# Optimization experiments

Measured on AMD Instinct MI355X. Metric: run time of the kernel, lower is better.

The kernel has to match this reference:

```python
import jax, jax.numpy as jnp
import numpy as np

N = 2048
D_MODEL = 1024
N_HEADS = 16
D_HEAD = D_MODEL // N_HEADS


def setup_inputs() -> dict:
    key = jax.random.key(0)
    ks = jax.random.split(key, 12)
    s = 1.0 / np.sqrt(D_MODEL)
    inp = {
        "x": jax.random.normal(ks[0], (N, D_MODEL), dtype=jnp.float32),
        "edge_bias": jax.random.normal(ks[1], (N, N, N_HEADS), dtype=jnp.float32) * 0.1,
        # torch.nn.Linear convention: y = x @ W.T + b, W: [out, in]
        "Wq": jax.random.normal(ks[2], (D_MODEL, D_MODEL), dtype=jnp.float32) * s,
        "bq": jax.random.normal(ks[3], (D_MODEL,), dtype=jnp.float32) * s,
        "Wk": jax.random.normal(ks[4], (D_MODEL, D_MODEL), dtype=jnp.float32) * s,
        "bk": jax.random.normal(ks[5], (D_MODEL,), dtype=jnp.float32) * s,
        "Wv": jax.random.normal(ks[6], (D_MODEL, D_MODEL), dtype=jnp.float32) * s,
        "bv": jax.random.normal(ks[7], (D_MODEL,), dtype=jnp.float32) * s,
        "Wo": jax.random.normal(ks[8], (D_MODEL, D_MODEL), dtype=jnp.float32) * s,
        "bo": jax.random.normal(ks[9], (D_MODEL,), dtype=jnp.float32) * s,
    }
    return inp


def reference(x, edge_bias, Wq, bq, Wk, bk, Wv, bv, Wo, bo):
    # x: [N, d], edge_bias: [N, N, H]
    scale = D_HEAD ** -0.5
    q = (x @ Wq.T + bq).reshape(N, N_HEADS, D_HEAD)  # [N, H, Dh]
    k = (x @ Wk.T + bk).reshape(N, N_HEADS, D_HEAD)
    v = (x @ Wv.T + bv).reshape(N, N_HEADS, D_HEAD)
    # attn[h, i, j] = q_i . k_j * scale + edge_bias[i, j, h]
    attn = jnp.einsum("nhd,mhd->hnm", q, k) * scale
    attn = attn + jnp.transpose(edge_bias, (2, 0, 1))
    attn = jax.nn.softmax(attn, axis=-1)
    # dropout is identity in eval/reference mode
    out = jnp.einsum("hnm,mhd->nhd", attn, v).reshape(N, D_MODEL)
    return out @ Wo.T + bo
```

## Files before the change

kernel.cpp:

```cpp
#include <hip/hip_runtime.h>
#include <math.h>

#define NTOK 2048
#define DM   1024
#define NH   16
#define DH   64
#define GM   2048
#define GN   1024
#define GK   1024
#define SCALE 0.125f

typedef __attribute__((ext_vector_type(8))) short short8;
typedef __attribute__((ext_vector_type(4))) float floatx4;
typedef unsigned short ushort_t;

__device__ __forceinline__ unsigned short f2bf(float f) {
    unsigned u = __builtin_bit_cast(unsigned, f);
    u += 0x7fffu + ((u >> 16) & 1u);
    return (unsigned short)(u >> 16);
}

__global__ __launch_bounds__(256) void convert5(
    const float* __restrict__ x,  const float* __restrict__ wq,
    const float* __restrict__ wk, const float* __restrict__ wv,
    const float* __restrict__ wo, ushort_t* __restrict__ dst)
{
    const size_t i4 = (size_t)blockIdx.x * 256 + threadIdx.x;
    const float* src; size_t off;
    if      (i4 <  524288) { src = x;  off = 0;       }
    else if (i4 <  786432) { src = wq; off = 524288;  }
    else if (i4 < 1048576) { src = wk; off = 786432;  }
    else if (i4 < 1310720) { src = wv; off = 1048576; }
    else                   { src = wo; off = 1310720; }
    float4 v = ((const float4*)src)[i4 - off];
    ushort4 o;
    o.x = f2bf(v.x); o.y = f2bf(v.y); o.z = f2bf(v.z); o.w = f2bf(v.w);
    ((ushort4*)dst)[i4] = o;
}

template<int BM, int BN>
__global__ __launch_bounds__(256) void gemm_bt(
    const ushort_t* __restrict__ A,
    const ushort_t* __restrict__ B0, const ushort_t* __restrict__ B1,
    const ushort_t* __restrict__ B2,
    const float* __restrict__ bi0, const float* __restrict__ bi1,
    const float* __restrict__ bi2,
    void* C0, void* C1, void* C2, int mode0, int mode1, int mode2)
{
    constexpr int AC = BM * 4 / 256;
    constexpr int BC = BN * 4 / 256;
    constexpr int FI = BM / 32;
    constexpr int FJ = BN / 32;
    constexpr int WM = BM / 2;
    constexpr int WN = BN / 2;

    const int z = blockIdx.z;
    const ushort_t* B   = (z == 0) ? B0  : (z == 1) ? B1  : B2;
    const float*    bia = (z == 0) ? bi0 : (z == 1) ? bi1 : bi2;
    void*           C   = (z == 0) ? C0  : (z == 1) ? C1  : C2;
    const int mode      = (z == 0) ? mode0 : (z == 1) ? mode1 : mode2;

    __shared__ __align__(16) ushort_t As[BM][32];
    __shared__ __align__(16) ushort_t Bs[BN][32];

    const int t    = threadIdx.x;
    const int w    = t >> 6;
    const int L    = t & 63;
    const int r16  = L & 15;
    const int quad = L >> 4;
    const int wm   = w & 1;
    const int wn   = w >> 1;

    const int m0 = blockIdx.y * BM;
    const int n0 = blockIdx.x * BN;

    const int srow = t >> 2;
    const int skc  = (t & 3) * 8;

    const ushort_t* ap = A + (size_t)(m0 + srow) * GK + skc;
    const ushort_t* bp = B + (size_t)(n0 + srow) * GK + skc;

    floatx4 acc[FI][FJ];
#pragma unroll
    for (int i = 0; i < FI; ++i)
#pragma unroll
        for (int j = 0; j < FJ; ++j) acc[i][j] = (floatx4){0.f, 0.f, 0.f, 0.f};

    short8 areg[AC], breg[BC];
#pragma unroll
    for (int c = 0; c < AC; ++c) areg[c] = *(const short8*)(ap + (size_t)c * 64 * GK);
#pragma unroll
    for (int c = 0; c < BC; ++c) breg[c] = *(const short8*)(bp + (size_t)c * 64 * GK);

    for (int ks = 0; ks < GK / 32; ++ks) {
        __syncthreads();
#pragma unroll
        for (int c = 0; c < AC; ++c) *(short8*)&As[c * 64 + srow][skc] = areg[c];
#pragma unroll
        for (int c = 0; c < BC; ++c) *(short8*)&Bs[c * 64 + srow][skc] = breg[c];
        __syncthreads();
        if (ks < GK / 32 - 1) {
            ap += 32; bp += 32;
#pragma unroll
            for (int c = 0; c < AC; ++c) areg[c] = *(const short8*)(ap + (size_t)c * 64 * GK);
#pragma unroll
            for (int c = 0; c < BC; ++c) breg[c] = *(const short8*)(bp + (size_t)c * 64 * GK);
        }
        short8 af[FI], bf[FJ];
#pragma unroll
        for (int fi = 0; fi < FI; ++fi)
            af[fi] = *(const short8*)&As[wm * WM + fi * 16 + r16][quad * 8];
#pragma unroll
        for (int fj = 0; fj < FJ; ++fj)
            bf[fj] = *(const short8*)&Bs[wn * WN + fj * 16 + r16][quad * 8];
#pragma unroll
        for (int fi = 0; fi < FI; ++fi)
#pragma unroll
            for (int fj = 0; fj < FJ; ++fj)
                acc[fi][fj] = __builtin_amdgcn_mfma_f32_16x16x32_bf16(
                    af[fi], bf[fj], acc[fi][fj], 0, 0, 0);
    }

#pragma unroll
    for (int fj = 0; fj < FJ; ++fj) {
        const int col = n0 + wn * WN + fj * 16 + r16;
        const float bv = bia[col];
#pragma unroll
        for (int fi = 0; fi < FI; ++fi) {
            const int row0 = m0 + wm * WM + fi * 16 + 4 * quad;
            floatx4 c = acc[fi][fj];
            if (mode == 2) {
                float* Cf = (float*)C;
#pragma unroll
                for (int i = 0; i < 4; ++i)
                    Cf[(size_t)(row0 + i) * GN + col] = c[i] + bv;
            } else if (mode == 0) {
                ushort_t* Cb = (ushort_t*)C;
#pragma unroll
                for (int i = 0; i < 4; ++i)
                    Cb[(size_t)(row0 + i) * GN + col] = f2bf(c[i] + bv);
            } else {
                ushort_t* Cb = (ushort_t*)C;
                ushort4 pk;
                pk.x = f2bf(c[0] + bv); pk.y = f2bf(c[1] + bv);
                pk.z = f2bf(c[2] + bv); pk.w = f2bf(c[3] + bv);
                *(ushort4*)(Cb + (size_t)col * GM + row0) = pk;
            }
        }
    }
}

#define NT   (NTOK / 32)
#define NCH  4
#define NTCH (NT / NCH)
#define JCH  (NTOK / NCH)
#define IB   32

__global__ __launch_bounds__(256) void attn4(
    const ushort_t* __restrict__ q, const ushort_t* __restrict__ k,
    const ushort_t* __restrict__ vT, const float* __restrict__ bias,
    float* __restrict__ opart, float* __restrict__ lpart)
{
    __shared__ float    Bb[2][4][IB][33];
    __shared__ ushort_t Ps[4][16][40];

    const int b    = blockIdx.x;
    const int ch   = blockIdx.y;
    const int jb   = ch * JCH;
    const int hg   = (b >> 3) & 3;
    const int it   = (b & 7) | ((b >> 5) << 3);
    const int i0   = it * IB;
    const int t    = threadIdx.x;
    const int w    = t >> 6;
    const int L    = t & 63;
    const int r16  = L & 15;
    const int quad = L >> 4;
    const int h    = hg * 4 + w;

#define kAddr(J0, JH, KC) (k  + (size_t)((J0) + (JH)*16 + r16) * DM + h*DH + (KC)*32 + quad*8)
#define vAddr(J0, DB)     (vT + (size_t)(h*DH + (DB)*16 + r16) * NTOK + (J0) + quad*8)
#define bAddr(J0, CI)     (bias + ((size_t)(i0 + (CI)*8 + (t>>5)) * NTOK + (J0) + (t&31)) * NH + hg*4)

    short8 qf[2][2];
#pragma unroll
    for (int r = 0; r < 2; ++r)
#pragma unroll
        for (int kc = 0; kc < 2; ++kc)
            qf[r][kc] = *(const short8*)(q + (size_t)(i0 + r * 16 + r16) * DM
                                           + h * DH + kc * 32 + quad * 8);

    short8 kf[2][4];
    short8 vf[2][4];
    float4 bst[4];

    bst[0] = *(const float4*)bAddr(jb, 0);
    bst[1] = *(const float4*)bAddr(jb, 1);
    bst[2] = *(const float4*)bAddr(jb, 2);
    bst[3] = *(const float4*)bAddr(jb, 3);
    kf[0][0] = *(const short8*)kAddr(jb, 0, 0);
    kf[0][1] = *(const short8*)kAddr(jb, 0, 1);
    kf[0][2] = *(const short8*)kAddr(jb, 1, 0);
    kf[0][3] = *(const short8*)kAddr(jb, 1, 1);
    vf[0][0] = *(const short8*)vAddr(jb, 0);
    vf[0][1] = *(const short8*)vAddr(jb, 1);
    vf[0][2] = *(const short8*)vAddr(jb, 2);
    vf[0][3] = *(const short8*)vAddr(jb, 3);
#pragma unroll
    for (int ci = 0; ci < 4; ++ci) {
        Bb[0][0][ci * 8 + (t >> 5)][t & 31] = bst[ci].x;
        Bb[0][1][ci * 8 + (t >> 5)][t & 31] = bst[ci].y;
        Bb[0][2][ci * 8 + (t >> 5)][t & 31] = bst[ci].z;
        Bb[0][3][ci * 8 + (t >> 5)][t & 31] = bst[ci].w;
    }
    __syncthreads();

    floatx4 o[2][4];
#pragma unroll
    for (int r = 0; r < 2; ++r)
#pragma unroll
        for (int d = 0; d < 4; ++d) o[r][d] = (floatx4){0.f, 0.f, 0.f, 0.f};
    float lrow[2][4] = {{0.f,0.f,0.f,0.f},{0.f,0.f,0.f,0.f}};

#define TILE(JT, CUR, NXT)                                                      \
  {                                                                             \
    const bool pre = (JT) < NTCH - 1;                                           \
    const int j0n = jb + ((JT) + 1) * 32;                                       \
    if (pre) {                                                                  \
      bst[0] = *(const float4*)bAddr(j0n, 0);                                   \
      bst[1] = *(const float4*)bAddr(j0n, 1);                                   \
      bst[2] = *(const float4*)bAddr(j0n, 2);                                   \
      bst[3] = *(const float4*)bAddr(j0n, 3);                                   \
      kf[NXT][0] = *(const short8*)kAddr(j0n, 0, 0);                            \
      kf[NXT][1] = *(const short8*)kAddr(j0n, 0, 1);                            \
      kf[NXT][2] = *(const short8*)kAddr(j0n, 1, 0);                            \
      kf[NXT][3] = *(const short8*)kAddr(j0n, 1, 1);                            \
      vf[NXT][0] = *(const short8*)vAddr(j0n, 0);                               \
      vf[NXT][1] = *(const short8*)vAddr(j0n, 1);                               \
      vf[NXT][2] = *(const short8*)vAddr(j0n, 2);                               \
      vf[NXT][3] = *(const short8*)vAddr(j0n, 3);                               \
    }                                                                           \
    floatx4 s00 = (floatx4){0.f,0.f,0.f,0.f};                                   \
    floatx4 s01 = (floatx4){0.f,0.f,0.f,0.f};                                   \
    floatx4 s10 = (floatx4){0.f,0.f,0.f,0.f};                                   \
    floatx4 s11 = (floatx4){0.f,0.f,0.f,0.f};                                   \
    s00 = __builtin_amdgcn_mfma_f32_16x16x32_bf16(qf[0][0], kf[CUR][0], s00, 0,0,0); \
    s00 = __builtin_amdgcn_mfma_f32_16x16x32_bf16(qf[0][1], kf[CUR][1], s00, 0,0,0); \
    s01 = __builtin_amdgcn_mfma_f32_16x16x32_bf16(qf[0][0], kf[CUR][2], s01, 0,0,0); \
    s01 = __builtin_amdgcn_mfma_f32_16x16x32_bf16(qf[0][1], kf[CUR][3], s01, 0,0,0); \
    s10 = __builtin_amdgcn_mfma_f32_16x16x32_bf16(qf[1][0], kf[CUR][0], s10, 0,0,0); \
    s10 = __builtin_amdgcn_mfma_f32_16x16x32_bf16(qf[1][1], kf[CUR][1], s10, 0,0,0); \
    s11 = __builtin_amdgcn_mfma_f32_16x16x32_bf16(qf[1][0], kf[CUR][2], s11, 0,0,0); \
    s11 = __builtin_amdgcn_mfma_f32_16x16x32_bf16(qf[1][1], kf[CUR][3], s11, 0,0,0); \
    _Pragma("unroll")                                                           \
    for (int ii = 0; ii < 4; ++ii) {                                            \
      const float bv0 = Bb[CUR][w][4 * quad + ii][r16];                         \
      const float bv1 = Bb[CUR][w][4 * quad + ii][16 + r16];                    \
      const float p0 = __expf(fmaf(s00[ii], SCALE, bv0));                       \
      const float p1 = __expf(fmaf(s01[ii], SCALE, bv1));                       \
      lrow[0][ii] += p0 + p1;                                                   \
      Ps[w][4 * quad + ii][r16]      = f2bf(p0);                                \
      Ps[w][4 * quad + ii][16 + r16] = f2bf(p1);                                \
    }                                                                           \
    {                                                                           \
      short8 pf = *(const short8*)&Ps[w][r16][quad * 8];                        \
      o[0][0] = __builtin_amdgcn_mfma_f32_16x16x32_bf16(pf, vf[CUR][0], o[0][0], 0,0,0); \
      o[0][1] = __builtin_amdgcn_mfma_f32_16x16x32_bf16(pf, vf[CUR][1], o[0][1], 0,0,0); \
      o[0][2] = __builtin_amdgcn_mfma_f32_16x16x32_bf16(pf, vf[CUR][2], o[0][2], 0,0,0); \
      o[0][3] = __builtin_amdgcn_mfma_f32_16x16x32_bf16(pf, vf[CUR][3], o[0][3], 0,0,0); \
    }                                                                           \
    _Pragma("unroll")                                                           \
    for (int ii = 0; ii < 4; ++ii) {                                            \
      const float bv0 = Bb[CUR][w][16 + 4 * quad + ii][r16];                    \
      const float bv1 = Bb[CUR][w][16 + 4 * quad + ii][16 + r16];               \
      const float p0 = __expf(fmaf(s10[ii], SCALE, bv0));                       \
      const float p1 = __expf(fmaf(s11[ii], SCALE, bv1));                       \
      lrow[1][ii] += p0 + p1;                                                   \
      Ps[w][4 * quad + ii][r16]      = f2bf(p0);                                \
      Ps[w][4 * quad + ii][16 + r16] = f2bf(p1);                                \
    }                                                                           \
    {                                                                           \
      short8 pf = *(const short8*)&Ps[w][r16][quad * 8];                        \
      o[1][0] = __builtin_amdgcn_mfma_f32_16x16x32_bf16(pf, vf[CUR][0], o[1][0], 0,0,0); \
      o[1][1] = __builtin_amdgcn_mfma_f32_16x16x32_bf16(pf, vf[CUR][1], o[1][1], 0,0,0); \
      o[1][2] = __builtin_amdgcn_mfma_f32_16x16x32_bf16(pf, vf[CUR][2], o[1][2], 0,0,0); \
      o[1][3] = __builtin_amdgcn_mfma_f32_16x16x32_bf16(pf, vf[CUR][3], o[1][3], 0,0,0); \
    }                                                                           \
    if (pre) {                                                                  \
      _Pragma("unroll")                                                         \
      for (int ci = 0; ci < 4; ++ci) {                                          \
        Bb[NXT][0][ci * 8 + (t >> 5)][t & 31] = bst[ci].x;                      \
        Bb[NXT][1][ci * 8 + (t >> 5)][t & 31] = bst[ci].y;                      \
        Bb[NXT][2][ci * 8 + (t >> 5)][t & 31] = bst[ci].z;                      \
        Bb[NXT][3][ci * 8 + (t >> 5)][t & 31] = bst[ci].w;                      \
      }                                                                         \
    }                                                                           \
    __syncthreads();                                                            \
  }

    for (int jt = 0; jt < NTCH; jt += 2) {
        TILE(jt, 0, 1)
        TILE(jt + 1, 1, 0)
    }

#pragma unroll
    for (int r = 0; r < 2; ++r) {
        float lred[4];
#pragma unroll
        for (int ii = 0; ii < 4; ++ii) {
            float s = lrow[r][ii];
#pragma unroll
            for (int d = 1; d < 16; d <<= 1) s += __shfl_xor(s, d);
            lred[ii] = s;
        }
        if (r16 == 0) {
#pragma unroll
            for (int ii = 0; ii < 4; ++ii)
                lpart[(size_t)ch * NH * NTOK + (size_t)h * NTOK
                      + i0 + r * 16 + 4 * quad + ii] = lred[ii];
        }
    }

    float* op = opart + (size_t)ch * NTOK * DM;
#pragma unroll
    for (int r = 0; r < 2; ++r)
#pragma unroll
        for (int db = 0; db < 4; ++db)
#pragma unroll
            for (int ii = 0; ii < 4; ++ii)
                op[(size_t)(i0 + r * 16 + 4 * quad + ii) * DM
                   + h * DH + db * 16 + r16] = o[r][db][ii];
#undef TILE
#undef kAddr
#undef vAddr
#undef bAddr
}

__global__ __launch_bounds__(256) void attn_fin(
    const float* __restrict__ opart, const float* __restrict__ lpart,
    ushort_t* __restrict__ ao)
{
    const int idx = blockIdx.x * 256 + threadIdx.x;
    const int n   = idx >> 8;
    const int d4  = idx & 255;
    const int h   = d4 >> 4;
    const size_t base = (size_t)n * DM + (size_t)d4 * 4;
    float4 s = {0.f, 0.f, 0.f, 0.f};
    float  l = 0.f;
#pragma unroll
    for (int c = 0; c < NCH; ++c) {
        float4 p = *(const float4*)(opart + (size_t)c * NTOK * DM + base);
        s.x += p.x; s.y += p.y; s.z += p.z; s.w += p.w;
        l += lpart[(size_t)c * NH * NTOK + (size_t)h * NTOK + n];
    }
    const float inv = 1.f / l;
    ushort4 o;
    o.x = f2bf(s.x * inv); o.y = f2bf(s.y * inv);
    o.z = f2bf(s.z * inv); o.w = f2bf(s.w * inv);
    ((ushort4*)ao)[idx] = o;
}

extern "C" void kernel_launch(void* const* d_in, const int* in_sizes, int n_in,
                              void* d_out, int out_size, void* d_ws, size_t ws_size,
                              hipStream_t stream)
{
    const float* x  = (const float*)d_in[0];
    const float* eb = (const float*)d_in[1];
    const float* Wq = (const float*)d_in[2];
    const float* bq = (const float*)d_in[3];
    const float* Wk = (const float*)d_in[4];
    const float* bk = (const float*)d_in[5];
    const float* Wv = (const float*)d_in[6];
    const float* bv = (const float*)d_in[7];
    const float* Wo = (const float*)d_in[8];
    const float* bo = (const float*)d_in[9];
    float* out = (float*)d_out;
    (void)in_sizes; (void)n_in; (void)out_size; (void)ws_size;

    const size_t E1 = (size_t)1024 * 1024;
    ushort_t* wsb = (ushort_t*)d_ws;
    ushort_t* xb  = wsb;
    ushort_t* Wqb = wsb + 2 * E1;
    ushort_t* Wkb = wsb + 3 * E1;
    ushort_t* Wvb = wsb + 4 * E1;
    ushort_t* Wob = wsb + 5 * E1;
    ushort_t* qb  = wsb + 6 * E1;
    ushort_t* kb  = wsb + 8 * E1;
    ushort_t* vTb = wsb + 10 * E1;
    ushort_t* aob = wsb + 12 * E1;
    float* opart = (float*)(wsb + 14 * E1);
    float* lpart = opart + (size_t)NCH * NTOK * DM;

    convert5<<<6144, 256, 0, stream>>>(x, Wq, Wk, Wv, Wo, wsb);

    {
        dim3 grid(GN / 64, GM / 128, 3);
        gemm_bt<128, 64><<<grid, 256, 0, stream>>>(
            xb, Wqb, Wkb, Wvb, bq, bk, bv,
            qb, kb, vTb, 0, 0, 1);
    }
    {
        dim3 grid((NTOK / IB) * 4, NCH, 1);
        attn4<<<grid, 256, 0, stream>>>(qb, kb, vTb, eb, opart, lpart);
    }
    attn_fin<<<NTOK * DM / 4 / 256, 256, 0, stream>>>(opart, lpart, aob);

    {
        dim3 grid(GN / 64, GM / 64, 1);
        gemm_bt<64, 64><<<grid, 256, 0, stream>>>(
            aob, Wob, Wob, Wob, bo, bo, bo,
            out, out, out, 2, 2, 2);
    }
}
```

Measured before the change: 496.3 us.

## Use direct global-to-LDS loads in GEMM and prefetch edge bias two tiles ahead

The GEMM mainloop stops staging A/B tiles through registers and issues global_load_lds, which writes 16-byte chunks straight into shared memory. In exchange it loses the register prefetch overlap, since loads are now issued and waited on within the same iteration. The attention kernel double-buffers the edge-bias registers and loads bias two tiles ahead, so more of the large bias stream's latency is hidden. That costs extra registers, which may lower occupancy.

```diff
diff --git a/kernel.cpp b/kernel.cpp
--- a/kernel.cpp
+++ b/kernel.cpp
@@ -19,6 +19,11 @@
     u += 0x7fffu + ((u >> 16) & 1u);
     return (unsigned short)(u >> 16);
 }
+
+#define GLOAD16(gsrc, ldst)                                                   \
+    __builtin_amdgcn_global_load_lds(                                         \
+        (const __attribute__((address_space(1))) unsigned int*)(gsrc),        \
+        (__attribute__((address_space(3))) unsigned int*)(ldst), 16, 0, 0)
 
 __global__ __launch_bounds__(256) void convert5(
     const float* __restrict__ x,  const float* __restrict__ wq,
@@ -65,9 +70,8 @@
 
     const int t    = threadIdx.x;
     const int w    = t >> 6;
-    const int L    = t & 63;
-    const int r16  = L & 15;
-    const int quad = L >> 4;
+    const int r16  = (t & 63) & 15;
+    const int quad = (t & 63) >> 4;
     const int wm   = w & 1;
     const int wn   = w >> 1;
 
@@ -86,26 +90,19 @@
 #pragma unroll
         for (int j = 0; j < FJ; ++j) acc[i][j] = (floatx4){0.f, 0.f, 0.f, 0.f};
 
-    short8 areg[AC], breg[BC];
-#pragma unroll
-    for (int c = 0; c < AC; ++c) areg[c] = *(const short8*)(ap + (size_t)c * 64 * GK);
-#pragma unroll
-    for (int c = 0; c < BC; ++c) breg[c] = *(const short8*)(bp + (size_t)c * 64 * GK);
-
     for (int ks = 0; ks < GK / 32; ++ks) {
         __syncthreads();
 #pragma unroll
-        for (int c = 0; c < AC; ++c) *(short8*)&As[c * 64 + srow][skc] = areg[c];
-#pragma unroll
-        for (int c = 0; c < BC; ++c) *(short8*)&Bs[c * 64 + srow][skc] = breg[c];
+        for (int c = 0; c < AC; ++c)
+            GLOAD16(ap + (size_t)c * 64 * GK,
+                    (ushort_t*)As + c * 2048 + w * 512);
+#pragma unroll
+        for (int c = 0; c < BC; ++c)
+            GLOAD16(bp + (size_t)c * 64 * GK,
+                    (ushort_t*)Bs + c * 2048 + w * 512);
+        ap += 32; bp += 32;
         __syncthreads();
-        if (ks < GK / 32 - 1) {
-            ap += 32; bp += 32;
-#pragma unroll
-            for (int c = 0; c < AC; ++c) areg[c] = *(const short8*)(ap + (size_t)c * 64 * GK);
-#pragma unroll
-            for (int c = 0; c < BC; ++c) breg[c] = *(const short8*)(bp + (size_t)c * 64 * GK);
-        }
+
         short8 af[FI], bf[FJ];
 #pragma unroll
         for (int fi = 0; fi < FI; ++fi)
@@ -191,12 +188,11 @@
 
     short8 kf[2][4];
     short8 vf[2][4];
-    float4 bst[4];
-
-    bst[0] = *(const float4*)bAddr(jb, 0);
-    bst[1] = *(const float4*)bAddr(jb, 1);
-    bst[2] = *(const float4*)bAddr(jb, 2);
-    bst[3] = *(const float4*)bAddr(jb, 3);
+    float4 bst[2][4];
+    float4 bpr[4];
+
+#pragma unroll
+    for (int ci = 0; ci < 4; ++ci) bpr[ci] = *(const float4*)bAddr(jb, ci);
     kf[0][0] = *(const short8*)kAddr(jb, 0, 0);
     kf[0][1] = *(const short8*)kAddr(jb, 0, 1);
     kf[0][2] = *(const short8*)kAddr(jb, 1, 0);
@@ -206,11 +202,13 @@
     vf[0][2] = *(const short8*)vAddr(jb, 2);
     vf[0][3] = *(const short8*)vAddr(jb, 3);
 #pragma unroll
+    for (int ci = 0; ci < 4; ++ci) bst[0][ci] = *(const float4*)bAddr(jb + 32, ci);
+#pragma unroll
     for (int ci = 0; ci < 4; ++ci) {
-        Bb[0][0][ci * 8 + (t >> 5)][t & 31] = bst[ci].x;
-        Bb[0][1][ci * 8 + (t >> 5)][t & 31] = bst[ci].y;
-        Bb[0][2][ci * 8 + (t >> 5)][t & 31] = bst[ci].z;
-        Bb[0][3][ci * 8 + (t >> 5)][t & 31] = bst[ci].w;
+        Bb[0][0][ci * 8 + (t >> 5)][t & 31] = bpr[ci].x;
+        Bb[0][1][ci * 8 + (t >> 5)][t & 31] = bpr[ci].y;
+        Bb[0][2][ci * 8 + (t >> 5)][t & 31] = bpr[ci].z;
+        Bb[0][3][ci * 8 + (t >> 5)][t & 31] = bpr[ci].w;
     }
     __syncthreads();
 
@@ -223,13 +221,11 @@
 
 #define TILE(JT, CUR, NXT)                                                      \
   {                                                                             \
-    const bool pre = (JT) < NTCH - 1;                                           \
+    const bool pre  = (JT) < NTCH - 1;                                          \
+    const bool pre2 = (JT) < NTCH - 2;                                          \
     const int j0n = jb + ((JT) + 1) * 32;                                       \
+    const int j0n2 = jb + ((JT) + 2) * 32;                                      \
     if (pre) {                                                                  \
-      bst[0] = *(const float4*)bAddr(j0n, 0);                                   \
-      bst[1] = *(const float4*)bAddr(j0n, 1);                                   \
-      bst[2] = *(const float4*)bAddr(j0n, 2);                                   \
-      bst[3] = *(const float4*)bAddr(j0n, 3);                                   \
       kf[NXT][0] = *(const short8*)kAddr(j0n, 0, 0);                            \
       kf[NXT][1] = *(const short8*)kAddr(j0n, 0, 1);                            \
       kf[NXT][2] = *(const short8*)kAddr(j0n, 1, 0);                            \
@@ -238,6 +234,12 @@
       vf[NXT][1] = *(const short8*)vAddr(j0n, 1);                               \
       vf[NXT][2] = *(const short8*)vAddr(j0n, 2);                               \
       vf[NXT][3] = *(const short8*)vAddr(j0n, 3);                               \
+    }                                                                           \
+    if (pre2) {                                                                 \
+      bst[NXT][0] = *(const float4*)bAddr(j0n2, 0);                             \
+      bst[NXT][1] = *(const float4*)bAddr(j0n2, 1);                             \
+      bst[NXT][2] = *(const float4*)bAddr(j0n2, 2);                             \
+      bst[NXT][3] = *(const float4*)bAddr(j0n2, 3);                             \
     }                                                                           \
     floatx4 s00 = (floatx4){0.f,0.f,0.f,0.f};                                   \
     floatx4 s01 = (floatx4){0.f,0.f,0.f,0.f};                                   \
@@ -288,10 +290,10 @@
     if (pre) {                                                                  \
       _Pragma("unroll")                                                         \
       for (int ci = 0; ci < 4; ++ci) {                                          \
-        Bb[NXT][0][ci * 8 + (t >> 5)][t & 31] = bst[ci].x;                      \
-        Bb[NXT][1][ci * 8 + (t >> 5)][t & 31] = bst[ci].y;                      \
-        Bb[NXT][2][ci * 8 + (t >> 5)][t & 31] = bst[ci].z;                      \
-        Bb[NXT][3][ci * 8 + (t >> 5)][t & 31] = bst[ci].w;                      \
+        Bb[NXT][0][ci * 8 + (t >> 5)][t & 31] = bst[CUR][ci].x;                 \
+        Bb[NXT][1][ci * 8 + (t >> 5)][t & 31] = bst[CUR][ci].y;                 \
+        Bb[NXT][2][ci * 8 + (t >> 5)][t & 31] = bst[CUR][ci].z;                 \
+        Bb[NXT][3][ci * 8 + (t >> 5)][t & 31] = bst[CUR][ci].w;                 \
       }                                                                         \
     }                                                                           \
     __syncthreads();                                                            \
```

Measured after the change: 496.4 us. Within noise of the previous version (+0.0%).
